# Kernel tuning notes

Measured on AMD Instinct MI355X. Metric: run time of the kernel, lower is better.

## Reference

```python
import jax, jax.numpy as jnp
import numpy as np

B, S, DIN, DOUT = 2, 2048, 4096, 4096


def setup_inputs() -> dict:
    key = jax.random.key(0)
    k1, k2 = jax.random.split(key)
    x = jax.random.normal(k1, (B, S, DIN), dtype=jnp.float32)
    weight = jax.random.normal(k2, (DOUT, DIN), dtype=jnp.float32) * 0.02
    # xnor init for row scaling pattern
    mean = weight.mean(-1, keepdims=True)                      # [DOUT,1]
    scale = jnp.abs(weight - mean).mean(-1, keepdims=True)     # [DOUT,1]
    wscale = scale
    wbias = mean
    return {"x": x, "weight": weight, "wscale": wscale, "wbias": wbias}


def reference(x, weight, wscale, wbias):
    # STE binarization: forward = sign(weight) (grad handled in bwd module)
    w_bin = jnp.sign(weight)
    w = wscale * w_bin + wbias                                 # [DOUT, DIN]
    # F.linear(x, w): x @ w.T, no bias
    out = jnp.einsum('bsk,nk->bsn', x, w)
    return out
```

## Files before the change

kernel.cpp:

```cpp
#include <hip/hip_runtime.h>
#include <stdint.h>


#define MDIM 4096
#define NDIM 4096
#define KDIM 4096

typedef int int4v  __attribute__((ext_vector_type(4)));
typedef int int16v __attribute__((ext_vector_type(16)));

__device__ __forceinline__ int pack4_rn(float a, float b, float c, float d, float inv) {
  int ia = __float2int_rn(a * inv) & 0xff;
  int ib = __float2int_rn(b * inv) & 0xff;
  int ic = __float2int_rn(c * inv) & 0xff;
  int id = __float2int_rn(d * inv) & 0xff;
  return ia | (ib << 8) | (ic << 16) | (id << 24);
}

__device__ __forceinline__ int sgn8(float v) {
  return (v > 0.f) ? 1 : ((v < 0.f) ? 0xff : 0);
}

#define PREP_XB 1024
#define PREP_WB 1024
__global__ __launch_bounds__(256) void prep_kernel(
    const float* __restrict__ x, const float* __restrict__ w,
    char* __restrict__ xq, char* __restrict__ wsg,
    float* __restrict__ xscale, float* __restrict__ sumx) {
  const int b = blockIdx.x;
  const int tid = threadIdx.x;
  const int lane = tid & 63, wv = tid >> 6;
  if (b < PREP_XB) {
    const int row = b * 4 + wv;
    const float4* xr = (const float4*)(x + (size_t)row * KDIM);
    float4 v[16];
    float s = 0.f, amax = 0.f;
#pragma unroll
    for (int u = 0; u < 16; ++u) {
      v[u] = xr[u * 64 + lane];
      s += v[u].x + v[u].y + v[u].z + v[u].w;
      amax = fmaxf(amax, fmaxf(fmaxf(fabsf(v[u].x), fabsf(v[u].y)),
                               fmaxf(fabsf(v[u].z), fabsf(v[u].w))));
    }
#pragma unroll
    for (int off = 32; off > 0; off >>= 1) {
      s += __shfl_xor(s, off, 64);
      amax = fmaxf(amax, __shfl_xor(amax, off, 64));
    }
    if (lane == 0) {
      sumx[row] = s;
      xscale[row] = amax * (1.f / 127.f);
    }
    const float inv = (amax > 0.f) ? 127.f / amax : 0.f;
    int* xo = (int*)(xq + (size_t)row * KDIM);
#pragma unroll
    for (int u = 0; u < 16; ++u)
      xo[u * 64 + lane] = pack4_rn(v[u].x, v[u].y, v[u].z, v[u].w, inv);
  } else {
    const float4* wr = (const float4*)w;
    int* wo = (int*)wsg;
    const size_t i0 = (size_t)(b - PREP_XB) * 256 + tid;
    const size_t stride = (size_t)PREP_WB * 256;
#pragma unroll
    for (int u = 0; u < 16; ++u) {
      size_t i = i0 + (size_t)u * stride;
      float4 vv = wr[i];
      wo[i] = sgn8(vv.x) | (sgn8(vv.y) << 8) | (sgn8(vv.z) << 16) | (sgn8(vv.w) << 24);
    }
  }
}

__global__ __launch_bounds__(512, 2) void gemm_bin_i8_m2(
    const char* __restrict__ A, const char* __restrict__ Bs,
    const float* __restrict__ wscale, const float* __restrict__ wbias,
    const float* __restrict__ xscale, const float* __restrict__ sumx,
    float* __restrict__ C) {
  __shared__ __align__(16) char sm[131072];

  const int bm = blockIdx.x >> 4, bn = blockIdx.x & 15;
  const int tm0 = bm * 256, tn0 = bn * 256;
  const int tid = threadIdx.x;
  const int lane = tid & 63, wave = tid >> 6;
  const int col32 = lane & 31, hl = lane >> 5;
  const int wr = wave >> 2, wc = wave & 3;

  int16v acc[4][2];
#pragma unroll
  for (int mi = 0; mi < 4; ++mi)
#pragma unroll
    for (int nj = 0; nj < 2; ++nj)
#pragma unroll
      for (int r = 0; r < 16; ++r) acc[mi][nj][r] = 0;

  int4v afA[8], bqA[4], afB[8], bqB[4];

  const int swc = (col32 >> 1) & 3;
  int baseA[2], baseB[2];
#pragma unroll
  for (int ks2 = 0; ks2 < 2; ++ks2) {
    baseA[ks2] = (wr * 128 + col32) * 64 + (((ks2 * 2 + hl) ^ swc) & 3) * 16;
    baseB[ks2] = (wc * 64 + col32) * 64 + (((ks2 * 2 + hl) ^ swc) & 3) * 16;
  }

  const int u0 = tid, u1 = tid + 512;
  const int r0 = u0 >> 2, r1 = u1 >> 2;
  const int c0 = (u0 & 3) ^ ((r0 >> 1) & 3);
  const int c1 = (u1 & 3) ^ ((r1 >> 1) & 3);
  const int offs0 = r0 * KDIM + c0 * 16;
  const int offs1 = r1 * KDIM + c1 * 16;
  const char* Abase = A + (size_t)tm0 * KDIM;
  const char* Bbase = Bs + (size_t)tn0 * KDIM;
  const int ldsu0 = tid * 16, ldsu1 = 8192 + tid * 16;

#define STAGE_AB(BUF, KH, KOFS)                                                   \
  do {                                                                            \
    const int sa_ = ((BUF) * 2 + (KH)) * 16384;                                   \
    const int sb_ = 65536 + sa_;                                                  \
    __builtin_amdgcn_global_load_lds(                                             \
        (const __attribute__((address_space(1))) void*)(Abase + offs0 + (KOFS)),  \
        (__attribute__((address_space(3))) void*)(sm + sa_ + ldsu0), 16, 0, 0);   \
    __builtin_amdgcn_global_load_lds(                                             \
        (const __attribute__((address_space(1))) void*)(Abase + offs1 + (KOFS)),  \
        (__attribute__((address_space(3))) void*)(sm + sa_ + ldsu1), 16, 0, 0);   \
    __builtin_amdgcn_global_load_lds(                                             \
        (const __attribute__((address_space(1))) void*)(Bbase + offs0 + (KOFS)),  \
        (__attribute__((address_space(3))) void*)(sm + sb_ + ldsu0), 16, 0, 0);   \
    __builtin_amdgcn_global_load_lds(                                             \
        (const __attribute__((address_space(1))) void*)(Bbase + offs1 + (KOFS)),  \
        (__attribute__((address_space(3))) void*)(sm + sb_ + ldsu1), 16, 0, 0);   \
  } while (0)

#define DSRD(SET, BUF, KS)                                                        \
  do {                                                                            \
    const int sa_ = ((BUF) * 2 + (KS)) * 16384;                                   \
    const int sb_ = 65536 + sa_;                                                  \
    _Pragma("unroll") for (int k2_ = 0; k2_ < 2; ++k2_) {                         \
      _Pragma("unroll") for (int mi_ = 0; mi_ < 4; ++mi_)                         \
          af##SET[k2_ * 4 + mi_] =                                                \
              *(const int4v*)(sm + sa_ + baseA[k2_] + mi_ * 2048);                \
      _Pragma("unroll") for (int nj_ = 0; nj_ < 2; ++nj_)                         \
          bq##SET[k2_ * 2 + nj_] =                                                \
              *(const int4v*)(sm + sb_ + baseB[k2_] + nj_ * 2048);                \
    }                                                                             \
  } while (0)

#define MFMA16(SET)                                                               \
  do {                                                                            \
    __builtin_amdgcn_s_setprio(1);                                                \
    _Pragma("unroll") for (int k2_ = 0; k2_ < 2; ++k2_)                           \
        _Pragma("unroll") for (int mi_ = 0; mi_ < 4; ++mi_)                       \
            _Pragma("unroll") for (int nj_ = 0; nj_ < 2; ++nj_)                   \
                acc[mi_][nj_] = __builtin_amdgcn_mfma_i32_32x32x32_i8(            \
                    af##SET[k2_ * 4 + mi_], bq##SET[k2_ * 2 + nj_],               \
                    acc[mi_][nj_], 0, 0, 0);                                      \
    __builtin_amdgcn_s_setprio(0);                                                \
  } while (0)

#define WAITL12                                                                   \
  do {                                                                            \
    asm volatile("s_waitcnt lgkmcnt(12)" ::: "memory");                           \
    __builtin_amdgcn_sched_barrier(0);                                            \
  } while (0)
#define WAITL0                                                                    \
  do {                                                                            \
    asm volatile("s_waitcnt lgkmcnt(0)" ::: "memory");                            \
    __builtin_amdgcn_sched_barrier(0);                                            \
  } while (0)

#define CKV4 asm volatile("s_waitcnt vmcnt(4)\n\ts_barrier" ::: "memory")
#define CKV0 asm volatile("s_waitcnt vmcnt(0)\n\ts_barrier" ::: "memory")

#define PHASE(CSET, NSET, NBUF, NKS, STAGEOP, ENDSYNC)                            \
  do {                                                                            \
    DSRD(NSET, NBUF, NKS);                                                        \
    STAGEOP;                                                                      \
    WAITL12;                                                                      \
    MFMA16(CSET);                                                                 \
    ENDSYNC;                                                                      \
  } while (0)

#define TILE_MAIN(BUF, TAU)                                                       \
  do {                                                                            \
    PHASE(A, B, BUF, 1, STAGE_AB((BUF) ^ 1, 1, ((TAU) + 1) * 128 + 64), CKV4);    \
    PHASE(B, A, (BUF) ^ 1, 0, STAGE_AB(BUF, 0, ((TAU) + 2) * 128), CKV4);         \
  } while (0)

  STAGE_AB(0, 0, 0);
  STAGE_AB(0, 1, 64);
  STAGE_AB(1, 0, 128);
  CKV4;
  DSRD(A, 0, 0);

#pragma unroll 1
  for (int t = 0; t < 30; t += 2) {
    TILE_MAIN(0, t);
    TILE_MAIN(1, t + 1);
  }

  PHASE(A, B, 0, 1, STAGE_AB(1, 1, 31 * 128 + 64), CKV4);
  PHASE(B, A, 1, 0, (void)0, CKV0);
  PHASE(A, B, 1, 1, (void)0, (void)0);
  WAITL0;
  MFMA16(B);

#undef TILE_MAIN
#undef PHASE
#undef CKV4
#undef CKV0
#undef WAITL12
#undef WAITL0
#undef MFMA16
#undef DSRD
#undef STAGE_AB

  float wsv[2], wbv[2];
#pragma unroll
  for (int nj = 0; nj < 2; ++nj) {
    int n = tn0 + wc * 64 + nj * 32 + col32;
    wsv[nj] = wscale[n];
    wbv[nj] = wbias[n];
  }
#pragma unroll
  for (int mi = 0; mi < 4; ++mi) {
#pragma unroll
    for (int reg = 0; reg < 16; ++reg) {
      int m = tm0 + wr * 128 + mi * 32 + (reg & 3) + 8 * (reg >> 2) + 4 * hl;
      float xs = xscale[m];
      float sx = sumx[m];
      float* crow = C + (size_t)m * NDIM + tn0 + wc * 64 + col32;
#pragma unroll
      for (int nj = 0; nj < 2; ++nj)
        crow[nj * 32] = wsv[nj] * xs * (float)acc[mi][nj][reg] + wbv[nj] * sx;
    }
  }
}

extern "C" void kernel_launch(void* const* d_in, const int* in_sizes, int n_in,
                              void* d_out, int out_size, void* d_ws, size_t ws_size,
                              hipStream_t stream) {
  const float* x      = (const float*)d_in[0];
  const float* weight = (const float*)d_in[1];
  const float* wscale = (const float*)d_in[2];
  const float* wbias  = (const float*)d_in[3];
  float* out = (float*)d_out;

  char* xq  = (char*)d_ws;
  char* wsg = xq + (size_t)MDIM * KDIM;
  float* xscale = (float*)(wsg + (size_t)NDIM * KDIM);
  float* sumx   = xscale + MDIM;

  prep_kernel<<<PREP_XB + PREP_WB, 256, 0, stream>>>(
      x, weight, xq, wsg, xscale, sumx);
  gemm_bin_i8_m2<<<(MDIM / 256) * (NDIM / 256), 512, 0, stream>>>(
      xq, wsg, wscale, wbias, xscale, sumx, out);
}
```

Baseline: 242.6 us.

## Shrink GEMM tile to 256x128 with four blocks per CU and XCD-aware mapping

Replaces the 256x256 tile, 128KB-LDS, two-blocks-per-CU int8 GEMM with a 256x128 tile that uses 48KB LDS and launch bounds of four blocks per CU. The k-step shrinks to 64 with simple double buffering and a full vmcnt(0) barrier each phase. Block indices are remapped so each XCD covers a contiguous group of tiles, aiming for better L2 reuse. The intent is to hide latency through more resident blocks rather than deep software pipelining, at the cost of less data reuse per tile and more frequent synchronisation.

Result: no change. 245.3 us (+1.1%).

```diff
diff --git a/kernel.cpp b/kernel.cpp
--- a/kernel.cpp
+++ b/kernel.cpp
@@ -70,148 +70,125 @@
   }
 }
 
-__global__ __launch_bounds__(512, 2) void gemm_bin_i8_m2(
+__global__ __launch_bounds__(512, 4) void gemm_bin_i8_cohab(
     const char* __restrict__ A, const char* __restrict__ Bs,
     const float* __restrict__ wscale, const float* __restrict__ wbias,
     const float* __restrict__ xscale, const float* __restrict__ sumx,
     float* __restrict__ C) {
-  __shared__ __align__(16) char sm[131072];
-
-  const int bm = blockIdx.x >> 4, bn = blockIdx.x & 15;
-  const int tm0 = bm * 256, tn0 = bn * 256;
+  __shared__ __align__(16) char sm[49152];
+
+  const int bid = blockIdx.x;
+  const int xcd = bid & 7, loc = bid >> 3;
+  const int bm = (xcd >> 1) * 4 + (loc >> 4);
+  const int bn = (xcd & 1) * 16 + (loc & 15);
+  const int tm0 = bm * 256, tn0 = bn * 128;
   const int tid = threadIdx.x;
   const int lane = tid & 63, wave = tid >> 6;
   const int col32 = lane & 31, hl = lane >> 5;
-  const int wr = wave >> 2, wc = wave & 3;
-
-  int16v acc[4][2];
-#pragma unroll
-  for (int mi = 0; mi < 4; ++mi)
+  const int wr = wave >> 1, wc = wave & 1;
+
+  int16v acc[2][2];
+#pragma unroll
+  for (int mi = 0; mi < 2; ++mi)
 #pragma unroll
     for (int nj = 0; nj < 2; ++nj)
 #pragma unroll
       for (int r = 0; r < 16; ++r) acc[mi][nj][r] = 0;
 
-  int4v afA[8], bqA[4], afB[8], bqB[4];
+  int4v af[4], bq[4];
 
   const int swc = (col32 >> 1) & 3;
-  int baseA[2], baseB[2];
+  int aBase[2], bBase[2];
 #pragma unroll
   for (int ks2 = 0; ks2 < 2; ++ks2) {
-    baseA[ks2] = (wr * 128 + col32) * 64 + (((ks2 * 2 + hl) ^ swc) & 3) * 16;
-    baseB[ks2] = (wc * 64 + col32) * 64 + (((ks2 * 2 + hl) ^ swc) & 3) * 16;
-  }
-
-  const int u0 = tid, u1 = tid + 512;
-  const int r0 = u0 >> 2, r1 = u1 >> 2;
-  const int c0 = (u0 & 3) ^ ((r0 >> 1) & 3);
-  const int c1 = (u1 & 3) ^ ((r1 >> 1) & 3);
-  const int offs0 = r0 * KDIM + c0 * 16;
-  const int offs1 = r1 * KDIM + c1 * 16;
+    aBase[ks2] = (wr * 64 + col32) * 64 + (((ks2 * 2 + hl) ^ swc) & 3) * 16;
+    bBase[ks2] = 32768 + (wc * 64 + col32) * 64 + (((ks2 * 2 + hl) ^ swc) & 3) * 16;
+  }
+
+  const int uA0 = tid, uA1 = tid + 512, uB = tid;
+  const int rA0 = uA0 >> 2, rA1 = uA1 >> 2, rB = uB >> 2;
+  const int offsA0 = rA0 * KDIM + (((uA0 & 3) ^ ((rA0 >> 1) & 3))) * 16;
+  const int offsA1 = rA1 * KDIM + (((uA1 & 3) ^ ((rA1 >> 1) & 3))) * 16;
+  const int offsB  = rB * KDIM + (((uB & 3) ^ ((rB >> 1) & 3))) * 16;
   const char* Abase = A + (size_t)tm0 * KDIM;
   const char* Bbase = Bs + (size_t)tn0 * KDIM;
-  const int ldsu0 = tid * 16, ldsu1 = 8192 + tid * 16;
-
-#define STAGE_AB(BUF, KH, KOFS)                                                   \
-  do {                                                                            \
-    const int sa_ = ((BUF) * 2 + (KH)) * 16384;                                   \
-    const int sb_ = 65536 + sa_;                                                  \
+  const int ldt = tid * 16;
+
+#define STAGE(BUF, KOFS)                                                          \
+  do {                                                                            \
+    const int sa_ = (BUF) * 16384;                                                \
+    const int sb_ = 32768 + (BUF) * 8192;                                         \
     __builtin_amdgcn_global_load_lds(                                             \
-        (const __attribute__((address_space(1))) void*)(Abase + offs0 + (KOFS)),  \
-        (__attribute__((address_space(3))) void*)(sm + sa_ + ldsu0), 16, 0, 0);   \
+        (const __attribute__((address_space(1))) void*)(Abase + offsA0 + (KOFS)), \
+        (__attribute__((address_space(3))) void*)(sm + sa_ + ldt), 16, 0, 0);     \
     __builtin_amdgcn_global_load_lds(                                             \
-        (const __attribute__((address_space(1))) void*)(Abase + offs1 + (KOFS)),  \
-        (__attribute__((address_space(3))) void*)(sm + sa_ + ldsu1), 16, 0, 0);   \
+        (const __attribute__((address_space(1))) void*)(Abase + offsA1 + (KOFS)), \
+        (__attribute__((address_space(3))) void*)(sm + sa_ + 8192 + ldt), 16, 0, 0);\
     __builtin_amdgcn_global_load_lds(                                             \
-        (const __attribute__((address_space(1))) void*)(Bbase + offs0 + (KOFS)),  \
-        (__attribute__((address_space(3))) void*)(sm + sb_ + ldsu0), 16, 0, 0);   \
-    __builtin_amdgcn_global_load_lds(                                             \
-        (const __attribute__((address_space(1))) void*)(Bbase + offs1 + (KOFS)),  \
-        (__attribute__((address_space(3))) void*)(sm + sb_ + ldsu1), 16, 0, 0);   \
-  } while (0)
-
-#define DSRD(SET, BUF, KS)                                                        \
-  do {                                                                            \
-    const int sa_ = ((BUF) * 2 + (KS)) * 16384;                                   \
-    const int sb_ = 65536 + sa_;                                                  \
-    _Pragma("unroll") for (int k2_ = 0; k2_ < 2; ++k2_) {                         \
-      _Pragma("unroll") for (int mi_ = 0; mi_ < 4; ++mi_)                         \
-          af##SET[k2_ * 4 + mi_] =                                                \
-              *(const int4v*)(sm + sa_ + baseA[k2_] + mi_ * 2048);                \
-      _Pragma("unroll") for (int nj_ = 0; nj_ < 2; ++nj_)                         \
-          bq##SET[k2_ * 2 + nj_] =                                                \
-              *(const int4v*)(sm + sb_ + baseB[k2_] + nj_ * 2048);                \
-    }                                                                             \
-  } while (0)
-
-#define MFMA16(SET)                                                               \
+        (const __attribute__((address_space(1))) void*)(Bbase + offsB + (KOFS)),  \
+        (__attribute__((address_space(3))) void*)(sm + sb_ + ldt), 16, 0, 0);     \
+  } while (0)
+
+#define DSRD(BUF)                                                                 \
+  do {                                                                            \
+    const int sa_ = (BUF) * 16384;                                                \
+    const int sb_ = (BUF) * 8192;                                                 \
+    af[0] = *(const int4v*)(sm + sa_ + aBase[0]);                                 \
+    af[1] = *(const int4v*)(sm + sa_ + aBase[0] + 2048);                          \
+    bq[0] = *(const int4v*)(sm + sb_ + bBase[0]);                                 \
+    bq[1] = *(const int4v*)(sm + sb_ + bBase[0] + 2048);                          \
+    af[2] = *(const int4v*)(sm + sa_ + aBase[1]);                                 \
+    af[3] = *(const int4v*)(sm + sa_ + aBase[1] + 2048);                          \
+    bq[2] = *(const int4v*)(sm + sb_ + bBase[1]);                                 \
+    bq[3] = *(const int4v*)(sm + sb_ + bBase[1] + 2048);                          \
+  } while (0)
+
+#define MFMA4(KS2)                                                                \
   do {                                                                            \
     __builtin_amdgcn_s_setprio(1);                                                \
-    _Pragma("unroll") for (int k2_ = 0; k2_ < 2; ++k2_)                           \
-        _Pragma("unroll") for (int mi_ = 0; mi_ < 4; ++mi_)                       \
-            _Pragma("unroll") for (int nj_ = 0; nj_ < 2; ++nj_)                   \
-                acc[mi_][nj_] = __builtin_amdgcn_mfma_i32_32x32x32_i8(            \
-                    af##SET[k2_ * 4 + mi_], bq##SET[k2_ * 2 + nj_],               \
-                    acc[mi_][nj_], 0, 0, 0);                                      \
+    _Pragma("unroll") for (int mi_ = 0; mi_ < 2; ++mi_)                           \
+        _Pragma("unroll") for (int nj_ = 0; nj_ < 2; ++nj_)                       \
+            acc[mi_][nj_] = __builtin_amdgcn_mfma_i32_32x32x32_i8(                \
+                af[(KS2) * 2 + mi_], bq[(KS2) * 2 + nj_], acc[mi_][nj_], 0, 0, 0);\
     __builtin_amdgcn_s_setprio(0);                                                \
   } while (0)
 
-#define WAITL12                                                                   \
-  do {                                                                            \
-    asm volatile("s_waitcnt lgkmcnt(12)" ::: "memory");                           \
+#define WAITL(N)                                                                  \
+  do {                                                                            \
+    asm volatile("s_waitcnt lgkmcnt(" #N ")" ::: "memory");                       \
     __builtin_amdgcn_sched_barrier(0);                                            \
   } while (0)
-#define WAITL0                                                                    \
-  do {                                                                            \
-    asm volatile("s_waitcnt lgkmcnt(0)" ::: "memory");                            \
-    __builtin_amdgcn_sched_barrier(0);                                            \
-  } while (0)
-
-#define CKV4 asm volatile("s_waitcnt vmcnt(4)\n\ts_barrier" ::: "memory")
+
 #define CKV0 asm volatile("s_waitcnt vmcnt(0)\n\ts_barrier" ::: "memory")
 
-#define PHASE(CSET, NSET, NBUF, NKS, STAGEOP, ENDSYNC)                            \
-  do {                                                                            \
-    DSRD(NSET, NBUF, NKS);                                                        \
+#define PHASE(BUF, STAGEOP, ENDSYNC)                                              \
+  do {                                                                            \
     STAGEOP;                                                                      \
-    WAITL12;                                                                      \
-    MFMA16(CSET);                                                                 \
+    DSRD(BUF);                                                                    \
+    WAITL(4);                                                                     \
+    MFMA4(0);                                                                     \
+    WAITL(0);                                                                     \
+    MFMA4(1);                                                                     \
     ENDSYNC;                                                                      \
   } while (0)
 
-#define TILE_MAIN(BUF, TAU)                                                       \
-  do {                                                                            \
-    PHASE(A, B, BUF, 1, STAGE_AB((BUF) ^ 1, 1, ((TAU) + 1) * 128 + 64), CKV4);    \
-    PHASE(B, A, (BUF) ^ 1, 0, STAGE_AB(BUF, 0, ((TAU) + 2) * 128), CKV4);         \
-  } while (0)
-
-  STAGE_AB(0, 0, 0);
-  STAGE_AB(0, 1, 64);
-  STAGE_AB(1, 0, 128);
-  CKV4;
-  DSRD(A, 0, 0);
+  STAGE(0, 0);
+  CKV0;
 
 #pragma unroll 1
-  for (int t = 0; t < 30; t += 2) {
-    TILE_MAIN(0, t);
-    TILE_MAIN(1, t + 1);
-  }
-
-  PHASE(A, B, 0, 1, STAGE_AB(1, 1, 31 * 128 + 64), CKV4);
-  PHASE(B, A, 1, 0, (void)0, CKV0);
-  PHASE(A, B, 1, 1, (void)0, (void)0);
-  WAITL0;
-  MFMA16(B);
-
-#undef TILE_MAIN
+  for (int t = 0; t < 62; t += 2) {
+    PHASE(0, STAGE(1, (t + 1) * 64), CKV0);
+    PHASE(1, STAGE(0, (t + 2) * 64), CKV0);
+  }
+  PHASE(0, STAGE(1, 63 * 64), CKV0);
+  PHASE(1, (void)0, (void)0);
+
 #undef PHASE
-#undef CKV4
 #undef CKV0
-#undef WAITL12
-#undef WAITL0
-#undef MFMA16
+#undef WAITL
+#undef MFMA4
 #undef DSRD
-#undef STAGE_AB
+#undef STAGE
 
   float wsv[2], wbv[2];
 #pragma unroll
@@ -221,10 +198,10 @@
     wbv[nj] = wbias[n];
   }
 #pragma unroll
-  for (int mi = 0; mi < 4; ++mi) {
+  for (int mi = 0; mi < 2; ++mi) {
 #pragma unroll
     for (int reg = 0; reg < 16; ++reg) {
-      int m = tm0 + wr * 128 + mi * 32 + (reg & 3) + 8 * (reg >> 2) + 4 * hl;
+      int m = tm0 + wr * 64 + mi * 32 + (reg & 3) + 8 * (reg >> 2) + 4 * hl;
       float xs = xscale[m];
       float sx = sumx[m];
       float* crow = C + (size_t)m * NDIM + tn0 + wc * 64 + col32;
@@ -251,6 +228,6 @@
 
   prep_kernel<<<PREP_XB + PREP_WB, 256, 0, stream>>>(
       x, weight, xq, wsg, xscale, sumx);
-  gemm_bin_i8_m2<<<(MDIM / 256) * (NDIM / 256), 512, 0, stream>>>(
+  gemm_bin_i8_cohab<<<(MDIM / 256) * (NDIM / 128), 512, 0, stream>>>(
       xq, wsg, wscale, wbias, xscale, sumx, out);
 }
```
